# Kernel tuning notes

Hardware: AMD Instinct MI355X
Metric: run time of the kernel (lower is better)

Reference implementation:

```python
import jax, jax.numpy as jnp
import numpy as np

B, S, HID = 2, 2048, 2048
NH, HD = 16, 128
EPS = 1e-5


def setup_inputs() -> dict:
    key = jax.random.key(0)
    ks = jax.random.split(key, 6)
    std = 1.0 / np.sqrt(HID)
    x = jax.random.normal(ks[0], (B, S, HID), dtype=jnp.float32)
    Wq = jax.random.normal(ks[1], (HID, NH * HD), dtype=jnp.float32) * std
    Wk = jax.random.normal(ks[2], (HID, NH * HD), dtype=jnp.float32) * std
    Wv = jax.random.normal(ks[3], (HID, NH * HD), dtype=jnp.float32) * std
    Wo = jax.random.normal(ks[4], (NH * HD, HID), dtype=jnp.float32) * std
    rms_w = jnp.ones((HID,), dtype=jnp.float32)
    # RoPE tables: freqs_cis.real / .imag, shape [S, HD//2]
    inv_freq = 1.0 / (10000.0 ** (np.arange(0, HD, 2, dtype=np.float32) / HD))
    angles = jnp.asarray(np.arange(S, dtype=np.float32)[:, None] * inv_freq[None, :])
    cos = jnp.cos(angles)
    sin = jnp.sin(angles)
    return {"x": x, "rms_w": rms_w, "Wq": Wq, "Wk": Wk, "Wv": Wv, "Wo": Wo,
            "cos": cos, "sin": sin}


def _rmsnorm(x, w):
    var = jnp.mean(jnp.square(x), axis=-1, keepdims=True)
    return x * jax.lax.rsqrt(var + EPS) * w


def _rope(t, cos, sin):
    # t: [B, S, H, D]; cos/sin: [S, D/2]  (rotate-half RoPE)
    d2 = t.shape[-1] // 2
    t1, t2 = t[..., :d2], t[..., d2:]
    c = cos[None, :, None, :]
    s = sin[None, :, None, :]
    return jnp.concatenate([t1 * c - t2 * s, t2 * c + t1 * s], axis=-1)


def reference(x, rms_w, Wq, Wk, Wv, Wo, cos, sin):
    residual = x
    h = _rmsnorm(x, rms_w)
    q = (h @ Wq).reshape(B, S, NH, HD)
    k = (h @ Wk).reshape(B, S, NH, HD)
    v = (h @ Wv).reshape(B, S, NH, HD)
    q = _rope(q, cos, sin)
    k = _rope(k, cos, sin)
    # [B, H, S, D]
    q = q.transpose(0, 2, 1, 3)
    k = k.transpose(0, 2, 1, 3)
    v = v.transpose(0, 2, 1, 3)
    scale = 1.0 / jnp.sqrt(jnp.float32(HD))
    scores = jnp.einsum('bhqd,bhkd->bhqk', q, k) * scale
    causal = jnp.tril(jnp.ones((S, S), dtype=bool))
    scores = jnp.where(causal[None, None], scores, jnp.finfo(scores.dtype).min)
    probs = jax.nn.softmax(scores, axis=-1)
    attn = jnp.einsum('bhqk,bhkd->bhqd', probs, v)
    attn = attn.transpose(0, 2, 1, 3).reshape(B, S, NH * HD)
    out = attn @ Wo
    return (residual + out).astype(x.dtype)
```

## Files before the change

### kernel.cpp

```cpp
#include <hip/hip_runtime.h>

#define HID   2048
#define S_LEN 2048
#define NHEAD 16
#define HD    128
#define NKV   2048

typedef __attribute__((ext_vector_type(8))) short   short8;
typedef __attribute__((ext_vector_type(4))) float   floatx4;

__device__ __forceinline__ unsigned short f2bf(float f) {
    union { float f; unsigned u; } v; v.f = f;
    unsigned r = v.u + 0x7fffu + ((v.u >> 16) & 1u);
    return (unsigned short)(r >> 16);
}
__device__ __forceinline__ float bf2f(unsigned short h) {
    union { unsigned u; float f; } v; v.u = ((unsigned)h) << 16; return v.f;
}

__device__ __forceinline__ void async16(void* lds, const void* g) {
    __builtin_amdgcn_global_load_lds(
        (const __attribute__((address_space(1))) unsigned int*)g,
        (__attribute__((address_space(3))) unsigned int*)lds, 16, 0, 0);
}

__global__ __launch_bounds__(256) void rmsnorm_kernel(const float* __restrict__ x,
        const float* __restrict__ w, unsigned short* __restrict__ h) {
    const int row = blockIdx.x;
    const int t = threadIdx.x;
    const float* xr = x + (size_t)row * HID;
    float4 v0 = *(const float4*)(xr + t * 4);
    float4 v1 = *(const float4*)(xr + 1024 + t * 4);
    float ss = v0.x*v0.x + v0.y*v0.y + v0.z*v0.z + v0.w*v0.w
             + v1.x*v1.x + v1.y*v1.y + v1.z*v1.z + v1.w*v1.w;
    #pragma unroll
    for (int off = 1; off < 64; off <<= 1) ss += __shfl_xor(ss, off, 64);
    __shared__ float red[4];
    if ((t & 63) == 0) red[t >> 6] = ss;
    __syncthreads();
    float tot = red[0] + red[1] + red[2] + red[3];
    float inv = rsqrtf(tot * (1.0f / HID) + 1e-5f);
    float4 w0 = *(const float4*)(w + t * 4);
    float4 w1 = *(const float4*)(w + 1024 + t * 4);
    ushort4 o0, o1;
    o0.x = f2bf(v0.x * inv * w0.x); o0.y = f2bf(v0.y * inv * w0.y);
    o0.z = f2bf(v0.z * inv * w0.z); o0.w = f2bf(v0.w * inv * w0.w);
    o1.x = f2bf(v1.x * inv * w1.x); o1.y = f2bf(v1.y * inv * w1.y);
    o1.z = f2bf(v1.z * inv * w1.z); o1.w = f2bf(v1.w * inv * w1.w);
    *(ushort4*)(h + (size_t)row * HID + t * 4) = o0;
    *(ushort4*)(h + (size_t)row * HID + 1024 + t * 4) = o1;
}

__global__ __launch_bounds__(256) void wtrans_kernel(const float* __restrict__ Wq,
        const float* __restrict__ Wk, const float* __restrict__ Wv,
        const float* __restrict__ Wo,
        unsigned short* __restrict__ wt_qkv, unsigned short* __restrict__ wt_o) {
    __shared__ float tile[64][65];
    const int sel = blockIdx.z;
    const float* W = (sel == 0) ? Wq : (sel == 1) ? Wk : (sel == 2) ? Wv : Wo;
    const int n0 = blockIdx.x * 64, k0 = blockIdx.y * 64;
    const int t = threadIdx.x;
    const int col = t & 63, r4 = t >> 6;
    #pragma unroll
    for (int i = 0; i < 16; ++i) {
        int rr = r4 + i * 4;
        tile[rr][col] = W[(size_t)(k0 + rr) * NKV + n0 + col];
    }
    __syncthreads();
    #pragma unroll
    for (int i = 0; i < 16; ++i) {
        int rr = r4 + i * 4;
        unsigned short v = f2bf(tile[col][rr]);
        if (sel < 3) wt_qkv[((size_t)(sel * 2048 + n0 + rr)) * HID + k0 + col] = v;
        else         wt_o  [((size_t)(n0 + rr)) * HID + k0 + col] = v;
    }
}

__device__ __forceinline__ void gemm_body(const unsigned short* __restrict__ A,
        const unsigned short* __restrict__ Bt, int K, int rowBase, int colBase,
        unsigned short* As, unsigned short* Bs, floatx4 acc[4][4]) {
    const int t = threadIdx.x;
    const int lane = t & 63, w = t >> 6;
    const int wm = (w >> 1) * 64, wn = (w & 1) * 64;
    const int lr = lane & 15, quad = lane >> 4;
    #pragma unroll
    for (int mi = 0; mi < 4; ++mi)
        #pragma unroll
        for (int ni = 0; ni < 4; ++ni) {
            acc[mi][ni][0] = 0.f; acc[mi][ni][1] = 0.f;
            acc[mi][ni][2] = 0.f; acc[mi][ni][3] = 0.f;
        }
    for (int k0 = 0; k0 < K; k0 += 64) {
        __syncthreads();
        #pragma unroll
        for (int c = 0; c < 4; ++c) {
            int e = (c * 256 + t) * 8;
            int r = e >> 6;
            int chunk = ((e >> 3) & 7) ^ (r & 7);
            async16(As + e, A  + (size_t)(rowBase + r) * K + k0 + chunk * 8);
            async16(Bs + e, Bt + (size_t)(colBase + r) * K + k0 + chunk * 8);
        }
        __syncthreads();
        #pragma unroll
        for (int ks = 0; ks < 2; ++ks) {
            short8 af[4], bfr[4];
            int cp = (ks * 4 + quad) ^ (lr & 7);
            #pragma unroll
            for (int i = 0; i < 4; ++i)
                af[i] = *(const short8*)(As + (wm + i * 16 + lr) * 64 + cp * 8);
            #pragma unroll
            for (int i = 0; i < 4; ++i)
                bfr[i] = *(const short8*)(Bs + (wn + i * 16 + lr) * 64 + cp * 8);
            #pragma unroll
            for (int mi = 0; mi < 4; ++mi)
                #pragma unroll
                for (int ni = 0; ni < 4; ++ni)
                    acc[mi][ni] = __builtin_amdgcn_mfma_f32_16x16x32_bf16(
                        af[mi], bfr[ni], acc[mi][ni], 0, 0, 0);
        }
    }
}

__global__ __launch_bounds__(256) void gemm_qkv_kernel(const unsigned short* __restrict__ h,
        const unsigned short* __restrict__ wt, unsigned short* __restrict__ qk,
        unsigned short* __restrict__ vT) {
    __shared__ __align__(16) unsigned short As[128 * 64];
    __shared__ __align__(16) unsigned short Bs[128 * 64];
    floatx4 acc[4][4];
    const int rowBase = blockIdx.y * 128, colBase = blockIdx.x * 128;
    gemm_body(h, wt, HID, rowBase, colBase, As, Bs, acc);
    const int t = threadIdx.x, lane = t & 63, w = t >> 6;
    const int wm = (w >> 1) * 64, wn = (w & 1) * 64;
    const int lr = lane & 15, quad = lane >> 4;
    const int sel = colBase >> 11;
    const int hh = (colBase >> 7) & 15;
    #pragma unroll
    for (int mi = 0; mi < 4; ++mi) {
        int row0 = rowBase + wm + mi * 16 + quad * 4;
        int b = row0 >> 11, s0 = row0 & 2047;
        #pragma unroll
        for (int ni = 0; ni < 4; ++ni) {
            int d = wn + ni * 16 + lr;
            if (sel < 2) {
                unsigned short* base = qk + (size_t)sel * 8388608
                                     + ((size_t)(b * NHEAD + hh) * S_LEN) * HD;
                #pragma unroll
                for (int r = 0; r < 4; ++r)
                    base[(size_t)(s0 + r) * HD + d] = f2bf(acc[mi][ni][r]);
            } else {
                ushort4 pk;
                pk.x = f2bf(acc[mi][ni][0]); pk.y = f2bf(acc[mi][ni][1]);
                pk.z = f2bf(acc[mi][ni][2]); pk.w = f2bf(acc[mi][ni][3]);
                *(ushort4*)(vT + ((size_t)(b * NHEAD + hh) * HD + d) * S_LEN + s0) = pk;
            }
        }
    }
}

__global__ __launch_bounds__(256) void rope_kernel(unsigned short* __restrict__ qk,
        const float* __restrict__ cosp, const float* __restrict__ sinp) {
    size_t idx = (size_t)blockIdx.x * 256 + threadIdx.x;
    int dp = idx & 63;
    size_t rowi = idx >> 6;
    int s = (int)(rowi & 2047);
    float c = cosp[s * 64 + dp], sn = sinp[s * 64 + dp];
    unsigned short* p = qk + rowi * 128;
    float t1 = bf2f(p[dp]), t2 = bf2f(p[dp + 64]);
    p[dp]      = f2bf(t1 * c - t2 * sn);
    p[dp + 64] = f2bf(t2 * c + t1 * sn);
}

__global__ __launch_bounds__(256, 2) void attn_kernel(const unsigned short* __restrict__ q,
        const unsigned short* __restrict__ k, const unsigned short* __restrict__ vT,
        unsigned short* __restrict__ out) {
    __shared__ __align__(16) unsigned short Kd[2][64 * 128];
    __shared__ __align__(16) unsigned short Vd[2][128 * 64];
    __shared__ __align__(16) unsigned short Ps[4][32 * 64];

    const int id = blockIdx.x;
    const int half = id >> 8;
    const int r8 = id & 255;
    const int bh = r8 >> 3;
    const int j  = r8 & 7;
    const int qi2 = half ? j : (15 - j);

    const unsigned short* qb = q  + (size_t)bh * S_LEN * HD;
    const unsigned short* kb = k  + (size_t)bh * S_LEN * HD;
    const unsigned short* vb = vT + (size_t)bh * HD * S_LEN;
    const int t = threadIdx.x, lane = t & 63, w = t >> 6;
    const int lr = lane & 15, quad = lane >> 4;

    short8 qf[2][4];
    #pragma unroll
    for (int mi = 0; mi < 2; ++mi) {
        int qrow = qi2 * 128 + mi * 64 + w * 16 + lr;
        #pragma unroll
        for (int ks = 0; ks < 4; ++ks)
            qf[mi][ks] = *(const short8*)(qb + (size_t)qrow * HD + ks * 32 + quad * 8);
    }
    floatx4 o[2][8];
    #pragma unroll
    for (int mi = 0; mi < 2; ++mi)
        #pragma unroll
        for (int i = 0; i < 8; ++i) { o[mi][i][0]=0.f; o[mi][i][1]=0.f; o[mi][i][2]=0.f; o[mi][i][3]=0.f; }
    float rs[2][4] = {{0.f,0.f,0.f,0.f},{0.f,0.f,0.f,0.f}};
    const float SC = 0.1275174855f;

    const int ktmax = 2 * qi2 + 1;

    auto stage = [&](int kt2, int buf) {
        unsigned short* Kb = &Kd[buf][0];
        unsigned short* Vb = &Vd[buf][0];
        #pragma unroll
        for (int c = 0; c < 4; ++c) {
            int e = (c * 256 + t) * 8;
            int kr = e >> 7;
            int kch = ((e >> 3) & 15) ^ (kr & 15);
            async16(Kb + e, kb + (size_t)(kt2 * 64 + kr) * HD + kch * 8);
            int vr = e >> 6;
            int vch = ((e >> 3) & 7) ^ (vr & 7);
            async16(Vb + e, vb + (size_t)vr * S_LEN + kt2 * 64 + vch * 8);
        }
    };

    stage(0, 0);

    for (int kt = 0; kt <= ktmax; ++kt) {
        __syncthreads();
        if (kt < ktmax) stage(kt + 1, (kt + 1) & 1);

        const unsigned short* Ksb = &Kd[kt & 1][0];
        const unsigned short* Vsb = &Vd[kt & 1][0];

        floatx4 sc[2][4];
        #pragma unroll
        for (int mi = 0; mi < 2; ++mi)
            #pragma unroll
            for (int ni = 0; ni < 4; ++ni) { sc[mi][ni][0]=0.f; sc[mi][ni][1]=0.f; sc[mi][ni][2]=0.f; sc[mi][ni][3]=0.f; }
        #pragma unroll
        for (int ks = 0; ks < 4; ++ks) {
            #pragma unroll
            for (int ni = 0; ni < 4; ++ni) {
                int row = ni * 16 + lr;
                int cp = (ks * 4 + quad) ^ (lr & 15);
                short8 kf = *(const short8*)(Ksb + row * 128 + cp * 8);
                sc[0][ni] = __builtin_amdgcn_mfma_f32_16x16x32_bf16(qf[0][ks], kf, sc[0][ni], 0, 0, 0);
                sc[1][ni] = __builtin_amdgcn_mfma_f32_16x16x32_bf16(qf[1][ks], kf, sc[1][ni], 0, 0, 0);
            }
        }

        const bool dtile = (kt >= 2 * qi2);
        #pragma unroll
        for (int mi = 0; mi < 2; ++mi) {
            int row_out = qi2 * 128 + mi * 64 + w * 16 + quad * 4;
            #pragma unroll
            for (int ni = 0; ni < 4; ++ni) {
                int key = kt * 64 + ni * 16 + lr;
                #pragma unroll
                for (int r = 0; r < 4; ++r) {
                    float p = exp2f(sc[mi][ni][r] * SC);
                    if (dtile && key > row_out + r) p = 0.f;
                    rs[mi][r] += p;
                    int prow = mi * 16 + quad * 4 + r;
                    int chunk = (ni * 2 + (lr >> 3)) ^ (prow & 7);
                    Ps[w][prow * 64 + chunk * 8 + (lr & 7)] = f2bf(p);
                }
            }
        }

        #pragma unroll
        for (int ks2 = 0; ks2 < 2; ++ks2) {
            int pcp = (ks2 * 4 + quad) ^ (lr & 7);
            short8 pa0 = *(const short8*)(&Ps[w][(lr) * 64 + pcp * 8]);
            short8 pa1 = *(const short8*)(&Ps[w][(16 + lr) * 64 + pcp * 8]);
            #pragma unroll
            for (int nt = 0; nt < 8; ++nt) {
                int row = nt * 16 + lr;
                int vcp = (ks2 * 4 + quad) ^ (lr & 7);
                short8 vf = *(const short8*)(Vsb + row * 64 + vcp * 8);
                o[0][nt] = __builtin_amdgcn_mfma_f32_16x16x32_bf16(pa0, vf, o[0][nt], 0, 0, 0);
                o[1][nt] = __builtin_amdgcn_mfma_f32_16x16x32_bf16(pa1, vf, o[1][nt], 0, 0, 0);
            }
        }
    }

    float rl[2][4];
    #pragma unroll
    for (int mi = 0; mi < 2; ++mi)
        #pragma unroll
        for (int r = 0; r < 4; ++r) {
            float s2 = rs[mi][r];
            #pragma unroll
            for (int off = 1; off < 16; off <<= 1) s2 += __shfl_xor(s2, off, 64);
            rl[mi][r] = 1.0f / s2;
        }
    const int b = bh >> 4, hh = bh & 15;
    #pragma unroll
    for (int mi = 0; mi < 2; ++mi) {
        size_t orow0 = (size_t)b * S_LEN + qi2 * 128 + mi * 64 + w * 16 + quad * 4;
        #pragma unroll
        for (int nt = 0; nt < 8; ++nt) {
            int col = hh * HD + nt * 16 + lr;
            #pragma unroll
            for (int r = 0; r < 4; ++r)
                out[(orow0 + r) * NKV + col] = f2bf(o[mi][nt][r] * rl[mi][r]);
        }
    }
}

__global__ __launch_bounds__(256) void gemm_out_kernel(const unsigned short* __restrict__ attn,
        const unsigned short* __restrict__ wto, const float* __restrict__ x,
        float* __restrict__ out) {
    __shared__ __align__(16) unsigned short As[128 * 64];
    __shared__ __align__(16) unsigned short Bs[128 * 64];
    floatx4 acc[4][4];
    const int rowBase = blockIdx.y * 128, colBase = blockIdx.x * 128;
    gemm_body(attn, wto, NKV, rowBase, colBase, As, Bs, acc);
    const int t = threadIdx.x, lane = t & 63, w = t >> 6;
    const int wm = (w >> 1) * 64, wn = (w & 1) * 64;
    const int lr = lane & 15, quad = lane >> 4;
    #pragma unroll
    for (int mi = 0; mi < 4; ++mi) {
        int row0 = rowBase + wm + mi * 16 + quad * 4;
        #pragma unroll
        for (int ni = 0; ni < 4; ++ni) {
            int col = colBase + wn + ni * 16 + lr;
            #pragma unroll
            for (int r = 0; r < 4; ++r) {
                size_t off = (size_t)(row0 + r) * HID + col;
                out[off] = acc[mi][ni][r] + x[off];
            }
        }
    }
}

extern "C" void kernel_launch(void* const* d_in, const int* in_sizes, int n_in,
                              void* d_out, int out_size, void* d_ws, size_t ws_size,
                              hipStream_t stream) {
    const float* x     = (const float*)d_in[0];
    const float* rms_w = (const float*)d_in[1];
    const float* Wq    = (const float*)d_in[2];
    const float* Wk    = (const float*)d_in[3];
    const float* Wv    = (const float*)d_in[4];
    const float* Wo    = (const float*)d_in[5];
    const float* cosp  = (const float*)d_in[6];
    const float* sinp  = (const float*)d_in[7];
    float* out = (float*)d_out;

    unsigned short* ws   = (unsigned short*)d_ws;
    unsigned short* h    = ws;
    unsigned short* wtq  = ws + 8388608;
    unsigned short* wto  = ws + 20971520;
    unsigned short* qk   = ws + 25165824;
    unsigned short* vT   = ws + 41943040;
    unsigned short* attn = ws + 50331648;

    rmsnorm_kernel<<<4096, 256, 0, stream>>>(x, rms_w, h);
    wtrans_kernel<<<dim3(32, 32, 4), 256, 0, stream>>>(Wq, Wk, Wv, Wo, wtq, wto);
    gemm_qkv_kernel<<<dim3(48, 32), 256, 0, stream>>>(h, wtq, qk, vT);
    rope_kernel<<<32768, 256, 0, stream>>>(qk, cosp, sinp);
    attn_kernel<<<512, 256, 0, stream>>>(qk, qk + 8388608, vT, attn);
    gemm_out_kernel<<<dim3(16, 32), 256, 0, stream>>>(attn, wto, x, out);
}
```

Baseline: 422.4 us.

## Fuse RoPE into QKV GEMM epilogue and specialize attention mask loop

Remaps each wave's N-columns in the GEMM so one thread holds both halves (d and d+64) of a head row, which lets RoPE run in the QKV GEMM epilogue and drops the separate rope kernel with its extra read and write of Q/K. The attention kernel now folds the softmax scale into Q when it loads Q, splits the key loop into unmasked and masked phases, and converts P to bf16 by truncation instead of rounding. This saves a launch and a memory pass. The cost is slightly different rounding, since Q is pre-scaled in bf16 and P is truncated.

```diff
diff --git a/kernel.cpp b/kernel.cpp
--- a/kernel.cpp
+++ b/kernel.cpp
@@ -81,7 +81,7 @@
         unsigned short* As, unsigned short* Bs, floatx4 acc[4][4]) {
     const int t = threadIdx.x;
     const int lane = t & 63, w = t >> 6;
-    const int wm = (w >> 1) * 64, wn = (w & 1) * 64;
+    const int wm = (w >> 1) * 64, wsel = w & 1;
     const int lr = lane & 15, quad = lane >> 4;
     #pragma unroll
     for (int mi = 0; mi < 4; ++mi)
@@ -110,7 +110,7 @@
                 af[i] = *(const short8*)(As + (wm + i * 16 + lr) * 64 + cp * 8);
             #pragma unroll
             for (int i = 0; i < 4; ++i)
-                bfr[i] = *(const short8*)(Bs + (wn + i * 16 + lr) * 64 + cp * 8);
+                bfr[i] = *(const short8*)(Bs + (i * 32 + wsel * 16 + lr) * 64 + cp * 8);
             #pragma unroll
             for (int mi = 0; mi < 4; ++mi)
                 #pragma unroll
@@ -122,7 +122,8 @@
 }
 
 __global__ __launch_bounds__(256) void gemm_qkv_kernel(const unsigned short* __restrict__ h,
-        const unsigned short* __restrict__ wt, unsigned short* __restrict__ qk,
+        const unsigned short* __restrict__ wt, const float* __restrict__ cosp,
+        const float* __restrict__ sinp, unsigned short* __restrict__ qk,
         unsigned short* __restrict__ vT) {
     __shared__ __align__(16) unsigned short As[128 * 64];
     __shared__ __align__(16) unsigned short Bs[128 * 64];
@@ -130,7 +131,7 @@
     const int rowBase = blockIdx.y * 128, colBase = blockIdx.x * 128;
     gemm_body(h, wt, HID, rowBase, colBase, As, Bs, acc);
     const int t = threadIdx.x, lane = t & 63, w = t >> 6;
-    const int wm = (w >> 1) * 64, wn = (w & 1) * 64;
+    const int wm = (w >> 1) * 64, wsel = w & 1;
     const int lr = lane & 15, quad = lane >> 4;
     const int sel = colBase >> 11;
     const int hh = (colBase >> 7) & 15;
@@ -138,16 +139,26 @@
     for (int mi = 0; mi < 4; ++mi) {
         int row0 = rowBase + wm + mi * 16 + quad * 4;
         int b = row0 >> 11, s0 = row0 & 2047;
-        #pragma unroll
-        for (int ni = 0; ni < 4; ++ni) {
-            int d = wn + ni * 16 + lr;
-            if (sel < 2) {
-                unsigned short* base = qk + (size_t)sel * 8388608
-                                     + ((size_t)(b * NHEAD + hh) * S_LEN) * HD;
+        if (sel < 2) {
+            unsigned short* base = qk + (size_t)sel * 8388608
+                                 + ((size_t)(b * NHEAD + hh) * S_LEN) * HD;
+            #pragma unroll
+            for (int ni = 0; ni < 2; ++ni) {
+                int d = ni * 32 + wsel * 16 + lr;
                 #pragma unroll
-                for (int r = 0; r < 4; ++r)
-                    base[(size_t)(s0 + r) * HD + d] = f2bf(acc[mi][ni][r]);
-            } else {
+                for (int r = 0; r < 4; ++r) {
+                    int s = s0 + r;
+                    float c  = cosp[s * 64 + d];
+                    float sn = sinp[s * 64 + d];
+                    float v1 = acc[mi][ni][r], v2 = acc[mi][ni + 2][r];
+                    base[(size_t)s * HD + d]      = f2bf(v1 * c - v2 * sn);
+                    base[(size_t)s * HD + d + 64] = f2bf(v2 * c + v1 * sn);
+                }
+            }
+        } else {
+            #pragma unroll
+            for (int ni = 0; ni < 4; ++ni) {
+                int d = ni * 32 + wsel * 16 + lr;
                 ushort4 pk;
                 pk.x = f2bf(acc[mi][ni][0]); pk.y = f2bf(acc[mi][ni][1]);
                 pk.z = f2bf(acc[mi][ni][2]); pk.w = f2bf(acc[mi][ni][3]);
@@ -155,19 +166,6 @@
             }
         }
     }
-}
-
-__global__ __launch_bounds__(256) void rope_kernel(unsigned short* __restrict__ qk,
-        const float* __restrict__ cosp, const float* __restrict__ sinp) {
-    size_t idx = (size_t)blockIdx.x * 256 + threadIdx.x;
-    int dp = idx & 63;
-    size_t rowi = idx >> 6;
-    int s = (int)(rowi & 2047);
-    float c = cosp[s * 64 + dp], sn = sinp[s * 64 + dp];
-    unsigned short* p = qk + rowi * 128;
-    float t1 = bf2f(p[dp]), t2 = bf2f(p[dp + 64]);
-    p[dp]      = f2bf(t1 * c - t2 * sn);
-    p[dp + 64] = f2bf(t2 * c + t1 * sn);
 }
 
 __global__ __launch_bounds__(256, 2) void attn_kernel(const unsigned short* __restrict__ q,
@@ -189,14 +187,19 @@
     const unsigned short* vb = vT + (size_t)bh * HD * S_LEN;
     const int t = threadIdx.x, lane = t & 63, w = t >> 6;
     const int lr = lane & 15, quad = lane >> 4;
+    const float SC = 0.1275174855f;
 
     short8 qf[2][4];
     #pragma unroll
     for (int mi = 0; mi < 2; ++mi) {
         int qrow = qi2 * 128 + mi * 64 + w * 16 + lr;
         #pragma unroll
-        for (int ks = 0; ks < 4; ++ks)
-            qf[mi][ks] = *(const short8*)(qb + (size_t)qrow * HD + ks * 32 + quad * 8);
+        for (int ks = 0; ks < 4; ++ks) {
+            short8 raw = *(const short8*)(qb + (size_t)qrow * HD + ks * 32 + quad * 8);
+            #pragma unroll
+            for (int jj = 0; jj < 8; ++jj)
+                qf[mi][ks][jj] = (short)f2bf(bf2f((unsigned short)raw[jj]) * SC);
+        }
     }
     floatx4 o[2][8];
     #pragma unroll
@@ -204,7 +207,6 @@
         #pragma unroll
         for (int i = 0; i < 8; ++i) { o[mi][i][0]=0.f; o[mi][i][1]=0.f; o[mi][i][2]=0.f; o[mi][i][3]=0.f; }
     float rs[2][4] = {{0.f,0.f,0.f,0.f},{0.f,0.f,0.f,0.f}};
-    const float SC = 0.1275174855f;
 
     const int ktmax = 2 * qi2 + 1;
 
@@ -223,15 +225,9 @@
         }
     };
 
-    stage(0, 0);
-
-    for (int kt = 0; kt <= ktmax; ++kt) {
-        __syncthreads();
-        if (kt < ktmax) stage(kt + 1, (kt + 1) & 1);
-
+    auto tilework = [&](int kt, bool maskf) {
         const unsigned short* Ksb = &Kd[kt & 1][0];
         const unsigned short* Vsb = &Vd[kt & 1][0];
-
         floatx4 sc[2][4];
         #pragma unroll
         for (int mi = 0; mi < 2; ++mi)
@@ -248,8 +244,6 @@
                 sc[1][ni] = __builtin_amdgcn_mfma_f32_16x16x32_bf16(qf[1][ks], kf, sc[1][ni], 0, 0, 0);
             }
         }
-
-        const bool dtile = (kt >= 2 * qi2);
         #pragma unroll
         for (int mi = 0; mi < 2; ++mi) {
             int row_out = qi2 * 128 + mi * 64 + w * 16 + quad * 4;
@@ -258,16 +252,16 @@
                 int key = kt * 64 + ni * 16 + lr;
                 #pragma unroll
                 for (int r = 0; r < 4; ++r) {
-                    float p = exp2f(sc[mi][ni][r] * SC);
-                    if (dtile && key > row_out + r) p = 0.f;
+                    float p = exp2f(sc[mi][ni][r]);
+                    if (maskf && key > row_out + r) p = 0.f;
                     rs[mi][r] += p;
                     int prow = mi * 16 + quad * 4 + r;
                     int chunk = (ni * 2 + (lr >> 3)) ^ (prow & 7);
-                    Ps[w][prow * 64 + chunk * 8 + (lr & 7)] = f2bf(p);
+                    Ps[w][prow * 64 + chunk * 8 + (lr & 7)] =
+                        (unsigned short)(__float_as_uint(p) >> 16);
                 }
             }
         }
-
         #pragma unroll
         for (int ks2 = 0; ks2 < 2; ++ks2) {
             int pcp = (ks2 * 4 + quad) ^ (lr & 7);
@@ -282,6 +276,19 @@
                 o[1][nt] = __builtin_amdgcn_mfma_f32_16x16x32_bf16(pa1, vf, o[1][nt], 0, 0, 0);
             }
         }
+    };
+
+    stage(0, 0);
+    int kt = 0;
+    for (; kt < 2 * qi2; ++kt) {
+        __syncthreads();
+        stage(kt + 1, (kt + 1) & 1);
+        tilework(kt, false);
+    }
+    for (; kt <= ktmax; ++kt) {
+        __syncthreads();
+        if (kt < ktmax) stage(kt + 1, (kt + 1) & 1);
+        tilework(kt, true);
     }
 
     float rl[2][4];
@@ -317,14 +324,14 @@
     const int rowBase = blockIdx.y * 128, colBase = blockIdx.x * 128;
     gemm_body(attn, wto, NKV, rowBase, colBase, As, Bs, acc);
     const int t = threadIdx.x, lane = t & 63, w = t >> 6;
-    const int wm = (w >> 1) * 64, wn = (w & 1) * 64;
+    const int wm = (w >> 1) * 64, wsel = w & 1;
     const int lr = lane & 15, quad = lane >> 4;
     #pragma unroll
     for (int mi = 0; mi < 4; ++mi) {
         int row0 = rowBase + wm + mi * 16 + quad * 4;
         #pragma unroll
         for (int ni = 0; ni < 4; ++ni) {
-            int col = colBase + wn + ni * 16 + lr;
+            int col = colBase + ni * 32 + wsel * 16 + lr;
             #pragma unroll
             for (int r = 0; r < 4; ++r) {
                 size_t off = (size_t)(row0 + r) * HID + col;
@@ -357,8 +364,7 @@
 
     rmsnorm_kernel<<<4096, 256, 0, stream>>>(x, rms_w, h);
     wtrans_kernel<<<dim3(32, 32, 4), 256, 0, stream>>>(Wq, Wk, Wv, Wo, wtq, wto);
-    gemm_qkv_kernel<<<dim3(48, 32), 256, 0, stream>>>(h, wtq, qk, vT);
-    rope_kernel<<<32768, 256, 0, stream>>>(qk, cosp, sinp);
+    gemm_qkv_kernel<<<dim3(48, 32), 256, 0, stream>>>(h, wtq, cosp, sinp, qk, vT);
     attn_kernel<<<512, 256, 0, stream>>>(qk, qk + 8388608, vT, attn);
     gemm_out_kernel<<<dim3(16, 32), 256, 0, stream>>>(attn, wto, x, out);
 }
```

Result: faster. 411.2 us (-2.6%).
